# Kernel optimization log

Measured on AMD Instinct MI355X. Metric: run time of the kernel, lower is better.

Reference implementation:

```python
import jax, jax.numpy as jnp
import numpy as np
import math

H = 8        # num_heads
D = 32       # dim_head
DEPTH = 1
LAMBDA_INIT = 0.8 - 0.6 * math.exp(-0.3 * DEPTH)
EPS = 1e-8


def setup_inputs() -> dict:
    key = jax.random.key(0)
    ks = jax.random.split(key, 9)
    B, T, IN_DIM, OUT_DIM = 2, 2048, 1024, 1024
    E = 2 * H * D  # 512
    inp = {
        "x": jax.random.normal(ks[0], (B, T, IN_DIM), dtype=jnp.float32),
        "Wq": jax.random.normal(ks[1], (IN_DIM, E), dtype=jnp.float32) * (IN_DIM ** -0.5),
        "Wkv": jax.random.normal(ks[2], (IN_DIM, 2 * E), dtype=jnp.float32) * (IN_DIM ** -0.5),
        "Wout": jax.random.normal(ks[3], (E, OUT_DIM), dtype=jnp.float32) * (E ** -0.5),
        "lambda_q1": 0.1 * jax.random.normal(ks[4], (D,), dtype=jnp.float32),
        "lambda_k1": 0.1 * jax.random.normal(ks[5], (D,), dtype=jnp.float32),
        "lambda_q2": 0.1 * jax.random.normal(ks[6], (D,), dtype=jnp.float32),
        "lambda_k2": 0.1 * jax.random.normal(ks[7], (D,), dtype=jnp.float32),
        "gamma": jnp.ones((2 * D,), dtype=jnp.float32),
    }
    return inp


def reference(x, Wq, Wkv, Wout, lambda_q1, lambda_k1, lambda_q2, lambda_k2, gamma):
    B, T, _ = x.shape
    scaling = D ** -0.5

    q = (x @ Wq).reshape(B, T, 2 * H, D).transpose(0, 2, 1, 3) * scaling  # [B,2H,T,D]
    kv = x @ Wkv
    k, v = jnp.split(kv, 2, axis=-1)
    k = k.reshape(B, T, 2 * H, D).transpose(0, 2, 1, 3)        # [B,2H,T,D]
    v = v.reshape(B, T, H, 2 * D).transpose(0, 2, 1, 3)        # [B,H,T,2D]

    dots = jnp.einsum('bhqd,bhkd->bhqk', q, k)                 # [B,2H,T,T]
    attn_w = jax.nn.softmax(dots.astype(jnp.float32), axis=-1).astype(dots.dtype)

    lam1 = jnp.exp(jnp.sum(lambda_q1 * lambda_k1))
    lam2 = jnp.exp(jnp.sum(lambda_q2 * lambda_k2))
    lam = lam1 - lam2 + LAMBDA_INIT

    attn_w = attn_w.reshape(B, H, 2, T, T)
    attn_w = attn_w[:, :, 0] - lam * attn_w[:, :, 1]           # [B,H,T,T]

    attn = jnp.einsum('bhqk,bhkd->bhqd', attn_w, v)            # [B,H,T,2D]

    rms = jnp.sqrt(jnp.mean(attn * attn, axis=-1, keepdims=True))
    attn = gamma * (attn / (rms + EPS))
    attn = attn * (1.0 - LAMBDA_INIT)

    attn = attn.transpose(0, 2, 1, 3).reshape(B, T, 2 * H * D)  # [B,T,E]
    return attn @ Wout
```

## Files before the change

kernel.cpp:

```cpp
#include <hip/hip_runtime.h>

typedef __attribute__((ext_vector_type(8)))  _Float16 half8;
typedef __attribute__((ext_vector_type(4)))  _Float16 half4;
typedef __attribute__((ext_vector_type(2)))  __fp16   fp16x2;
typedef __attribute__((ext_vector_type(4)))  float    f32x4;

#define MFMA16(a,b,c) __builtin_amdgcn_mfma_f32_16x16x32_f16(a,b,c,0,0,0)

#define QSCALE       0.17677669529663687f
#define LAMBDA_INIT  0.3555090675909693f
#define OUT_SCALE    0.6444909324090307f
#define LOG2E        1.4426950408889634f
#define MSHIFT       4.0f

#define EXP2(x) __builtin_amdgcn_exp2f(x)

__device__ __forceinline__ void gld16(const void* g, void* l) {
    __builtin_amdgcn_global_load_lds(
        (const __attribute__((address_space(1))) unsigned int*)g,
        (__attribute__((address_space(3))) unsigned int*)l, 16, 0, 0);
}

__device__ __forceinline__ void tr64(const float* __restrict__ src,
                                     _Float16* __restrict__ dst,
                                     int srcld, int dstld, int bx, int by) {
    __shared__ float t[64][65];
    int k0 = bx * 64, n0 = by * 64;
    int c = threadIdx.x & 63, rr = threadIdx.x >> 6;
#pragma unroll
    for (int ph = 0; ph < 16; ++ph) {
        int k = ph * 4 + rr;
        t[k][c] = src[(size_t)(k0 + k) * srcld + n0 + c];
    }
    __syncthreads();
#pragma unroll
    for (int ph = 0; ph < 16; ++ph) {
        int n = ph * 4 + rr;
        dst[(size_t)(n0 + n) * dstld + k0 + c] = (_Float16)t[c][n];
    }
}

__global__ __launch_bounds__(256) void k_prep(const float* __restrict__ x,
                                              const float* __restrict__ Wq,
                                              const float* __restrict__ Wkv,
                                              const float* __restrict__ Wout,
                                              _Float16* __restrict__ xh,
                                              _Float16* __restrict__ WallT,
                                              _Float16* __restrict__ WoutT) {
    int b = blockIdx.x;
    if (b < 4096) {
        int i = (b * 256 + threadIdx.x) * 4;
        f32x4 v = *(const f32x4*)(x + i);
        half4 h;
        h[0] = (_Float16)v[0]; h[1] = (_Float16)v[1];
        h[2] = (_Float16)v[2]; h[3] = (_Float16)v[3];
        *(half4*)(xh + i) = h;
    } else if (b < 4224) {
        int idx = b - 4096;
        tr64(Wq, WallT, 512, 1024, idx & 15, idx >> 4);
    } else if (b < 4480) {
        int idx = b - 4224;
        tr64(Wkv, WallT + 512 * 1024, 1024, 1024, idx & 15, idx >> 4);
    } else {
        int idx = b - 4480;
        tr64(Wout, WoutT, 1024, 512, idx & 7, idx >> 3);
    }
}

__device__ __forceinline__ void gemm_loop(const _Float16* __restrict__ A,
                                          const _Float16* __restrict__ Bt,
                                          int K, int bm, int bn,
                                          char* As, char* Bs,
                                          f32x4 (&acc)[4][4]) {
    int tid = threadIdx.x, lane = tid & 63, w = tid >> 6;
    int col16 = lane & 15, quad = lane >> 4;
    int wm = (w >> 1) << 6, wn = (w & 1) << 6;
    int r0 = tid >> 2;
    int kc = (tid & 3) << 3;
    const _Float16* ga0 = A  + (size_t)(bm + r0) * K + kc;
    const _Float16* ga1 = A  + (size_t)(bm + 64 + r0) * K + kc;
    const _Float16* gb0 = Bt + (size_t)(bn + r0) * K + kc;
    const _Float16* gb1 = Bt + (size_t)(bn + 64 + r0) * K + kc;
    char* lA = As + (w << 10);
    char* lB = Bs + (w << 10);

    gld16(ga0, lA);
    gld16(ga1, lA + 4096);
    gld16(gb0, lB);
    gld16(gb1, lB + 4096);

    for (int k0 = 0; k0 < K; k0 += 32) {
        __syncthreads();
        int cb = (k0 >> 5) & 1;
        if (k0 + 32 < K) {
            int nb = (cb ^ 1) << 13;
            gld16(ga0 + k0 + 32, lA + nb);
            gld16(ga1 + k0 + 32, lA + nb + 4096);
            gld16(gb0 + k0 + 32, lB + nb);
            gld16(gb1 + k0 + 32, lB + nb + 4096);
        }
        const char* Asc = As + (cb << 13);
        const char* Bsc = Bs + (cb << 13);
        half8 af[4], bf[4];
#pragma unroll
        for (int i = 0; i < 4; ++i)
            af[i] = *(const half8*)(Asc + ((wm + i * 16 + col16) << 6) + (quad << 4));
#pragma unroll
        for (int j = 0; j < 4; ++j)
            bf[j] = *(const half8*)(Bsc + ((wn + j * 16 + col16) << 6) + (quad << 4));
#pragma unroll
        for (int i = 0; i < 4; ++i)
#pragma unroll
            for (int j = 0; j < 4; ++j)
                acc[i][j] = MFMA16(af[i], bf[j], acc[i][j]);
    }
}

__global__ __launch_bounds__(256) void k_gemm_qkv(const _Float16* __restrict__ xh,
                                                  const _Float16* __restrict__ WallT,
                                                  _Float16* __restrict__ qbuf,
                                                  char* __restrict__ Kf,
                                                  char* __restrict__ Vf) {
    __shared__ __align__(16) char As[16384];
    __shared__ __align__(16) char Bs[16384];
    f32x4 acc[4][4] = {};
    int bm = blockIdx.x * 128, bn = blockIdx.y * 128;
    gemm_loop(xh, WallT, 1024, bm, bn, As, Bs, acc);

    int tid = threadIdx.x, lane = tid & 63, w = tid >> 6;
    int col16 = lane & 15, quad = lane >> 4;
    int wm = (w >> 1) << 6, wn = (w & 1) << 6;

    if (bn < 512) {
        const float s = QSCALE * LOG2E;
#pragma unroll
        for (int i = 0; i < 4; ++i)
#pragma unroll
            for (int j = 0; j < 4; ++j) {
                int n = bn + wn + j * 16 + col16;
                int m0 = bm + wm + i * 16 + quad * 4;
#pragma unroll
                for (int r = 0; r < 4; ++r)
                    qbuf[(size_t)(m0 + r) * 512 + n] = (_Float16)(acc[i][j][r] * s);
            }
    } else if (bn < 1024) {
#pragma unroll
        for (int j = 0; j < 4; ++j) {
            int n = bn + wn + j * 16 + col16 - 512;
            int pp = n >> 6, dd = n & 63, head = dd >> 5, d32 = dd & 31;
            int lbase = (d32 >> 3) << 4;
            int e2 = (d32 & 7) << 1;
            int fragb = head << 11;
#pragma unroll
            for (int i = 0; i < 4; ++i) {
                int m0 = bm + wm + i * 16 + quad * 4;
                int b = m0 >> 11, tok = m0 & 2047, kb = tok >> 5, kk = tok & 31;
                char* dst = Kf + (((size_t)((b * 8 + pp) * 64 + kb)) << 12)
                          + fragb + ((kk >> 4) << 10) + ((lbase + (kk & 15)) << 4) + e2;
#pragma unroll
                for (int r = 0; r < 4; ++r)
                    *(_Float16*)(dst + (r << 4)) = (_Float16)acc[i][j][r];
            }
        }
    } else {
#pragma unroll
        for (int j = 0; j < 4; ++j) {
            int n = bn + wn + j * 16 + col16 - 1024;
            int pp = n >> 6, ch = n & 63;
            int off_t = ((ch >> 4) << 10) + ((ch & 15) << 4);
#pragma unroll
            for (int i = 0; i < 4; ++i) {
                int m0 = bm + wm + i * 16 + quad * 4;
                int b = m0 >> 11, tok = m0 & 2047, kb = tok >> 5, kk = tok & 31;
                int quadv = (kk < 16) ? (kk >> 2) : ((kk - 16) >> 2);
                int e0 = (kk < 16) ? 0 : 4;
                half4 hv;
#pragma unroll
                for (int r = 0; r < 4; ++r) hv[r] = (_Float16)acc[i][j][r];
                *(half4*)(Vf + (((size_t)((b * 8 + pp) * 64 + kb)) << 12)
                          + off_t + (quadv << 8) + (e0 << 1)) = hv;
            }
        }
    }
}

__global__ __launch_bounds__(512, 4) void k_attn_fused(
        const _Float16* __restrict__ qbuf,
        const char* __restrict__ Kf,
        const char* __restrict__ Vf,
        const float* __restrict__ lq1,
        const float* __restrict__ lk1,
        const float* __restrict__ lq2,
        const float* __restrict__ lk2,
        const float* __restrict__ gamma,
        _Float16* __restrict__ attnO) {
    __shared__ __align__(16) char Sh[2][32768];
    __shared__ float Ls[2][8][16];

    int blk = blockIdx.x;
    int r32 = blk & 63, p = (blk >> 6) & 7, bb = blk >> 9;
    int tid = threadIdx.x, lane = tid & 63, w = tid >> 6;
    int qt2 = w & 1, c = w >> 1;
    int col16 = lane & 15, quad = lane >> 4;

    int qrow = bb * 2048 + r32 * 32 + qt2 * 16 + col16;
    const _Float16* qb = qbuf + (size_t)qrow * 512 + p * 64;
    half8 q1 = *(const half8*)(qb + quad * 8);
    half8 q2 = *(const half8*)(qb + 32 + quad * 8);

    size_t bpoff = ((size_t)(bb * 8 + p)) << 18;
    const char* src2 = ((tid >= 256) ? Vf : Kf) + bpoff + ((tid & 255) << 4);
    int dbase = ((tid >= 256) ? 4096 : 0) + ((tid & 255) << 4);

    const f32x4 minit = {-MSHIFT, -MSHIFT, -MSHIFT, -MSHIFT};

    float l1 = 0.f, l2 = 0.f;
    f32x4 o1[4] = {}, o2[4] = {};

#pragma unroll
    for (int j = 0; j < 4; ++j)
        gld16(src2 + ((size_t)(j << 4) << 12), (char*)Sh + (j << 13) + dbase);

    for (int it = 0; it < 16; ++it) {
        __syncthreads();
        if (it + 1 < 16) {
#pragma unroll
            for (int j = 0; j < 4; ++j)
                gld16(src2 + ((size_t)((j << 4) + it + 1) << 12),
                      (char*)Sh + (((it + 1) & 1) << 15) + (j << 13) + dbase);
        }
        const char* kvb = (char*)Sh + ((it & 1) << 15) + (c << 13) + (lane << 4);

        half8 kf0 = *(const half8*)(kvb);
        half8 kf1 = *(const half8*)(kvb + 1024);
        half8 kf2 = *(const half8*)(kvb + 2048);
        half8 kf3 = *(const half8*)(kvb + 3072);
        f32x4 sa1 = MFMA16(kf0, q1, minit), sb1 = MFMA16(kf1, q1, minit);
        f32x4 sa2 = MFMA16(kf2, q2, minit), sb2 = MFMA16(kf3, q2, minit);

        union { half8 v; fp16x2 h[4]; } p1u, p2u;
        {
            float a0 = EXP2(sa1[0]), a1 = EXP2(sa1[1]);
            float a2 = EXP2(sa1[2]), a3 = EXP2(sa1[3]);
            float b0 = EXP2(sb1[0]), b1 = EXP2(sb1[1]);
            float b2 = EXP2(sb1[2]), b3 = EXP2(sb1[3]);
            l1 += ((a0 + a1) + (a2 + a3)) + ((b0 + b1) + (b2 + b3));
            p1u.h[0] = __builtin_amdgcn_cvt_pkrtz(a0, a1);
            p1u.h[1] = __builtin_amdgcn_cvt_pkrtz(a2, a3);
            p1u.h[2] = __builtin_amdgcn_cvt_pkrtz(b0, b1);
            p1u.h[3] = __builtin_amdgcn_cvt_pkrtz(b2, b3);
        }
        {
            float a0 = EXP2(sa2[0]), a1 = EXP2(sa2[1]);
            float a2 = EXP2(sa2[2]), a3 = EXP2(sa2[3]);
            float b0 = EXP2(sb2[0]), b1 = EXP2(sb2[1]);
            float b2 = EXP2(sb2[2]), b3 = EXP2(sb2[3]);
            l2 += ((a0 + a1) + (a2 + a3)) + ((b0 + b1) + (b2 + b3));
            p2u.h[0] = __builtin_amdgcn_cvt_pkrtz(a0, a1);
            p2u.h[1] = __builtin_amdgcn_cvt_pkrtz(a2, a3);
            p2u.h[2] = __builtin_amdgcn_cvt_pkrtz(b0, b1);
            p2u.h[3] = __builtin_amdgcn_cvt_pkrtz(b2, b3);
        }
        half8 vf0 = *(const half8*)(kvb + 4096);
        half8 vf1 = *(const half8*)(kvb + 5120);
        half8 vf2 = *(const half8*)(kvb + 6144);
        half8 vf3 = *(const half8*)(kvb + 7168);
        o1[0] = MFMA16(p1u.v, vf0, o1[0]); o2[0] = MFMA16(p2u.v, vf0, o2[0]);
        o1[1] = MFMA16(p1u.v, vf1, o1[1]); o2[1] = MFMA16(p2u.v, vf1, o2[1]);
        o1[2] = MFMA16(p1u.v, vf2, o1[2]); o2[2] = MFMA16(p2u.v, vf2, o2[2]);
        o1[3] = MFMA16(p1u.v, vf3, o1[3]); o2[3] = MFMA16(p2u.v, vf3, o2[3]);
    }

    l1 += __shfl_xor(l1, 16); l1 += __shfl_xor(l1, 32);
    l2 += __shfl_xor(l2, 16); l2 += __shfl_xor(l2, 32);

    {
        _Float16* ob = (_Float16*)((char*)Sh + ((c * 2 + qt2) << 12)) + col16;
#pragma unroll
        for (int r = 0; r < 4; ++r) {
            _Float16* od = ob + (quad * 4 + r) * 128;
#pragma unroll
            for (int t = 0; t < 4; ++t) {
                od[t * 16]      = (_Float16)o1[t][r];
                od[64 + t * 16] = (_Float16)o2[t][r];
            }
        }
        if (quad == 0) { Ls[0][w][col16] = l1; Ls[1][w][col16] = l2; }
    }
    __syncthreads();

    int rr = tid >> 4, jj = tid & 15;
    int qrt = rr >> 4, r16 = rr & 15;
    float o1s[4] = {}, o2s[4] = {};
    float l1s = 0.f, l2s = 0.f;
#pragma unroll
    for (int cc = 0; cc < 4; ++cc) {
        const _Float16* ob = (const _Float16*)((char*)Sh + ((cc * 2 + qrt) << 12))
                           + r16 * 128 + jj * 4;
        half4 a  = *(const half4*)ob;
        half4 b2 = *(const half4*)(ob + 64);
#pragma unroll
        for (int e = 0; e < 4; ++e) { o1s[e] += (float)a[e]; o2s[e] += (float)b2[e]; }
        l1s += Ls[0][cc * 2 + qrt][r16];
        l2s += Ls[1][cc * 2 + qrt][r16];
    }
    float s1 = 0.f, s2 = 0.f;
#pragma unroll
    for (int i = 0; i < 32; ++i) { s1 += lq1[i] * lk1[i]; s2 += lq2[i] * lk2[i]; }
    float lam = __expf(s1) - __expf(s2) + LAMBDA_INIT;
    float il1 = 1.f / l1s, il2 = lam / l2s;
    float Of[4], ss = 0.f;
#pragma unroll
    for (int e = 0; e < 4; ++e) { Of[e] = o1s[e] * il1 - o2s[e] * il2; ss += Of[e] * Of[e]; }
    ss += __shfl_xor(ss, 1, 16); ss += __shfl_xor(ss, 2, 16);
    ss += __shfl_xor(ss, 4, 16); ss += __shfl_xor(ss, 8, 16);
    float rms = sqrtf(ss * 0.015625f);
    float sc = OUT_SCALE / (rms + 1e-8f);
    half4 o;
#pragma unroll
    for (int e = 0; e < 4; ++e) o[e] = (_Float16)(gamma[jj * 4 + e] * Of[e] * sc);
    *(half4*)(attnO + ((size_t)(bb * 2048 + r32 * 32 + rr) * 512) + p * 64 + jj * 4) = o;
}

__global__ __launch_bounds__(256) void k_gemm_out(const _Float16* __restrict__ attn,
                                                  const _Float16* __restrict__ WoutT,
                                                  float* __restrict__ out) {
    __shared__ __align__(16) char As[16384];
    __shared__ __align__(16) char Bs[16384];
    f32x4 acc[4][4] = {};
    int bm = blockIdx.x * 128, bn = blockIdx.y * 128;
    gemm_loop(attn, WoutT, 512, bm, bn, As, Bs, acc);

    int tid = threadIdx.x, lane = tid & 63, w = tid >> 6;
    int col16 = lane & 15, quad = lane >> 4;
    int wm = (w >> 1) << 6, wn = (w & 1) << 6;
#pragma unroll
    for (int i = 0; i < 4; ++i)
#pragma unroll
        for (int j = 0; j < 4; ++j) {
            int n = bn + wn + j * 16 + col16;
            int m0 = bm + wm + i * 16 + quad * 4;
#pragma unroll
            for (int r = 0; r < 4; ++r)
                out[(size_t)(m0 + r) * 1024 + n] = acc[i][j][r];
        }
}

extern "C" void kernel_launch(void* const* d_in, const int* in_sizes, int n_in,
                              void* d_out, int out_size, void* d_ws, size_t ws_size,
                              hipStream_t stream) {
    const float* x     = (const float*)d_in[0];
    const float* Wq    = (const float*)d_in[1];
    const float* Wkv   = (const float*)d_in[2];
    const float* Wout  = (const float*)d_in[3];
    const float* lq1   = (const float*)d_in[4];
    const float* lk1   = (const float*)d_in[5];
    const float* lq2   = (const float*)d_in[6];
    const float* lk2   = (const float*)d_in[7];
    const float* gamma = (const float*)d_in[8];
    float* out = (float*)d_out;

    char* ws = (char*)d_ws;
    _Float16* xh    = (_Float16*)(ws);
    _Float16* WallT = (_Float16*)(ws + 8388608);
    _Float16* WoutT = (_Float16*)(ws + 11534336);
    _Float16* qbuf  = (_Float16*)(ws + 12582912);
    char*     Kf    = (char*)(ws + 16777216);
    char*     Vf    = (char*)(ws + 20971520);
    _Float16* attn  = (_Float16*)(ws + 25165824);

    k_prep<<<4608, 256, 0, stream>>>(x, Wq, Wkv, Wout, xh, WallT, WoutT);
    k_gemm_qkv<<<dim3(32, 12), 256, 0, stream>>>(xh, WallT, qbuf, Kf, Vf);
    k_attn_fused<<<1024, 512, 0, stream>>>(qbuf, Kf, Vf, lq1, lk1, lq2, lk2, gamma, attn);
    k_gemm_out<<<dim3(32, 8), 256, 0, stream>>>(attn, WoutT, out);
}
```

Baseline: 168.9 us.

## Load V directly from global to registers, stage only K in LDS, remap blocks

V fragments are now read straight from global memory into registers instead of being staged through LDS. The freed LDS holds twice as many K tiles per stage, so the loop runs 8 iterations over two K sub-tiles each. Block indices are also reordered so that consecutive blocks span different batch/head pairs, which changes the L2 access pattern. The intent is fewer barriers and less LDS traffic per key. The risk is global-load latency on V that is now exposed, plus more registers in use.

After: 175.5 us. 1.04x slower.

```diff
diff --git a/kernel.cpp b/kernel.cpp
--- a/kernel.cpp
+++ b/kernel.cpp
@@ -198,7 +198,9 @@
     __shared__ float Ls[2][8][16];
 
     int blk = blockIdx.x;
-    int r32 = blk & 63, p = (blk >> 6) & 7, bb = blk >> 9;
+    int bp  = ((blk & 7) << 1) | ((blk >> 3) & 1);
+    int r32 = blk >> 4;
+    int p = bp & 7, bb = bp >> 3;
     int tid = threadIdx.x, lane = tid & 63, w = tid >> 6;
     int qt2 = w & 1, c = w >> 1;
     int col16 = lane & 15, quad = lane >> 4;
@@ -209,8 +211,12 @@
     half8 q2 = *(const half8*)(qb + 32 + quad * 8);
 
     size_t bpoff = ((size_t)(bb * 8 + p)) << 18;
-    const char* src2 = ((tid >= 256) ? Vf : Kf) + bpoff + ((tid & 255) << 4);
-    int dbase = ((tid >= 256) ? 4096 : 0) + ((tid & 255) << 4);
+    int j = tid >> 7;
+    int toff = (tid & 127) << 4;
+    const char* ks = Kf + bpoff + ((size_t)j << 16) + toff;
+    int dko = (j << 13) + toff;
+
+    const char* vsrc = Vf + bpoff + ((size_t)c << 16) + (lane << 4);
 
     const f32x4 minit = {-MSHIFT, -MSHIFT, -MSHIFT, -MSHIFT};
 
@@ -218,62 +224,103 @@
     f32x4 o1[4] = {}, o2[4] = {};
 
 #pragma unroll
-    for (int j = 0; j < 4; ++j)
-        gld16(src2 + ((size_t)(j << 4) << 12), (char*)Sh + (j << 13) + dbase);
-
-    for (int it = 0; it < 16; ++it) {
+    for (int r = 0; r < 4; ++r)
+        gld16(ks + r * 2048, (char*)Sh + dko + r * 2048);
+
+    for (int it = 0; it < 8; ++it) {
         __syncthreads();
-        if (it + 1 < 16) {
-#pragma unroll
-            for (int j = 0; j < 4; ++j)
-                gld16(src2 + ((size_t)((j << 4) + it + 1) << 12),
-                      (char*)Sh + (((it + 1) & 1) << 15) + (j << 13) + dbase);
+
+        half8 vA0 = *(const half8*)(vsrc);
+        half8 vA1 = *(const half8*)(vsrc + 1024);
+        half8 vA2 = *(const half8*)(vsrc + 2048);
+        half8 vA3 = *(const half8*)(vsrc + 3072);
+        half8 vB0 = *(const half8*)(vsrc + 4096);
+        half8 vB1 = *(const half8*)(vsrc + 5120);
+        half8 vB2 = *(const half8*)(vsrc + 6144);
+        half8 vB3 = *(const half8*)(vsrc + 7168);
+        vsrc += 8192;
+
+        if (it + 1 < 8) {
+            char* d = (char*)Sh + (((it + 1) & 1) << 15) + dko;
+            const char* s = ks + ((size_t)(it + 1) << 13);
+#pragma unroll
+            for (int r = 0; r < 4; ++r)
+                gld16(s + r * 2048, d + r * 2048);
         }
         const char* kvb = (char*)Sh + ((it & 1) << 15) + (c << 13) + (lane << 4);
 
-        half8 kf0 = *(const half8*)(kvb);
-        half8 kf1 = *(const half8*)(kvb + 1024);
-        half8 kf2 = *(const half8*)(kvb + 2048);
-        half8 kf3 = *(const half8*)(kvb + 3072);
-        f32x4 sa1 = MFMA16(kf0, q1, minit), sb1 = MFMA16(kf1, q1, minit);
-        f32x4 sa2 = MFMA16(kf2, q2, minit), sb2 = MFMA16(kf3, q2, minit);
-
-        union { half8 v; fp16x2 h[4]; } p1u, p2u;
+        half8 ka0 = *(const half8*)(kvb);
+        half8 ka1 = *(const half8*)(kvb + 1024);
+        half8 ka2 = *(const half8*)(kvb + 2048);
+        half8 ka3 = *(const half8*)(kvb + 3072);
+        f32x4 saA1 = MFMA16(ka0, q1, minit), sbA1 = MFMA16(ka1, q1, minit);
+        f32x4 saA2 = MFMA16(ka2, q2, minit), sbA2 = MFMA16(ka3, q2, minit);
+        half8 kb0 = *(const half8*)(kvb + 4096);
+        half8 kb1 = *(const half8*)(kvb + 5120);
+        half8 kb2 = *(const half8*)(kvb + 6144);
+        half8 kb3 = *(const half8*)(kvb + 7168);
+        f32x4 saB1 = MFMA16(kb0, q1, minit), sbB1 = MFMA16(kb1, q1, minit);
+        f32x4 saB2 = MFMA16(kb2, q2, minit), sbB2 = MFMA16(kb3, q2, minit);
+
+        union { half8 v; fp16x2 h[4]; } pA1, pA2, pB1, pB2;
         {
-            float a0 = EXP2(sa1[0]), a1 = EXP2(sa1[1]);
-            float a2 = EXP2(sa1[2]), a3 = EXP2(sa1[3]);
-            float b0 = EXP2(sb1[0]), b1 = EXP2(sb1[1]);
-            float b2 = EXP2(sb1[2]), b3 = EXP2(sb1[3]);
+            float a0 = EXP2(saA1[0]), a1 = EXP2(saA1[1]);
+            float a2 = EXP2(saA1[2]), a3 = EXP2(saA1[3]);
+            float b0 = EXP2(sbA1[0]), b1 = EXP2(sbA1[1]);
+            float b2 = EXP2(sbA1[2]), b3 = EXP2(sbA1[3]);
             l1 += ((a0 + a1) + (a2 + a3)) + ((b0 + b1) + (b2 + b3));
-            p1u.h[0] = __builtin_amdgcn_cvt_pkrtz(a0, a1);
-            p1u.h[1] = __builtin_amdgcn_cvt_pkrtz(a2, a3);
-            p1u.h[2] = __builtin_amdgcn_cvt_pkrtz(b0, b1);
-            p1u.h[3] = __builtin_amdgcn_cvt_pkrtz(b2, b3);
+            pA1.h[0] = __builtin_amdgcn_cvt_pkrtz(a0, a1);
+            pA1.h[1] = __builtin_amdgcn_cvt_pkrtz(a2, a3);
+            pA1.h[2] = __builtin_amdgcn_cvt_pkrtz(b0, b1);
+            pA1.h[3] = __builtin_amdgcn_cvt_pkrtz(b2, b3);
         }
         {
-            float a0 = EXP2(sa2[0]), a1 = EXP2(sa2[1]);
-            float a2 = EXP2(sa2[2]), a3 = EXP2(sa2[3]);
-            float b0 = EXP2(sb2[0]), b1 = EXP2(sb2[1]);
-            float b2 = EXP2(sb2[2]), b3 = EXP2(sb2[3]);
+            float a0 = EXP2(saA2[0]), a1 = EXP2(saA2[1]);
+            float a2 = EXP2(saA2[2]), a3 = EXP2(saA2[3]);
+            float b0 = EXP2(sbA2[0]), b1 = EXP2(sbA2[1]);
+            float b2 = EXP2(sbA2[2]), b3 = EXP2(sbA2[3]);
             l2 += ((a0 + a1) + (a2 + a3)) + ((b0 + b1) + (b2 + b3));
-            p2u.h[0] = __builtin_amdgcn_cvt_pkrtz(a0, a1);
-            p2u.h[1] = __builtin_amdgcn_cvt_pkrtz(a2, a3);
-            p2u.h[2] = __builtin_amdgcn_cvt_pkrtz(b0, b1);
-            p2u.h[3] = __builtin_amdgcn_cvt_pkrtz(b2, b3);
-        }
-        half8 vf0 = *(const half8*)(kvb + 4096);
-        half8 vf1 = *(const half8*)(kvb + 5120);
-        half8 vf2 = *(const half8*)(kvb + 6144);
-        half8 vf3 = *(const half8*)(kvb + 7168);
-        o1[0] = MFMA16(p1u.v, vf0, o1[0]); o2[0] = MFMA16(p2u.v, vf0, o2[0]);
-        o1[1] = MFMA16(p1u.v, vf1, o1[1]); o2[1] = MFMA16(p2u.v, vf1, o2[1]);
-        o1[2] = MFMA16(p1u.v, vf2, o1[2]); o2[2] = MFMA16(p2u.v, vf2, o2[2]);
-        o1[3] = MFMA16(p1u.v, vf3, o1[3]); o2[3] = MFMA16(p2u.v, vf3, o2[3]);
+            pA2.h[0] = __builtin_amdgcn_cvt_pkrtz(a0, a1);
+            pA2.h[1] = __builtin_amdgcn_cvt_pkrtz(a2, a3);
+            pA2.h[2] = __builtin_amdgcn_cvt_pkrtz(b0, b1);
+            pA2.h[3] = __builtin_amdgcn_cvt_pkrtz(b2, b3);
+        }
+        o1[0] = MFMA16(pA1.v, vA0, o1[0]); o2[0] = MFMA16(pA2.v, vA0, o2[0]);
+        o1[1] = MFMA16(pA1.v, vA1, o1[1]); o2[1] = MFMA16(pA2.v, vA1, o2[1]);
+        o1[2] = MFMA16(pA1.v, vA2, o1[2]); o2[2] = MFMA16(pA2.v, vA2, o2[2]);
+        o1[3] = MFMA16(pA1.v, vA3, o1[3]); o2[3] = MFMA16(pA2.v, vA3, o2[3]);
+        {
+            float a0 = EXP2(saB1[0]), a1 = EXP2(saB1[1]);
+            float a2 = EXP2(saB1[2]), a3 = EXP2(saB1[3]);
+            float b0 = EXP2(sbB1[0]), b1 = EXP2(sbB1[1]);
+            float b2 = EXP2(sbB1[2]), b3 = EXP2(sbB1[3]);
+            l1 += ((a0 + a1) + (a2 + a3)) + ((b0 + b1) + (b2 + b3));
+            pB1.h[0] = __builtin_amdgcn_cvt_pkrtz(a0, a1);
+            pB1.h[1] = __builtin_amdgcn_cvt_pkrtz(a2, a3);
+            pB1.h[2] = __builtin_amdgcn_cvt_pkrtz(b0, b1);
+            pB1.h[3] = __builtin_amdgcn_cvt_pkrtz(b2, b3);
+        }
+        {
+            float a0 = EXP2(saB2[0]), a1 = EXP2(saB2[1]);
+            float a2 = EXP2(saB2[2]), a3 = EXP2(saB2[3]);
+            float b0 = EXP2(sbB2[0]), b1 = EXP2(sbB2[1]);
+            float b2 = EXP2(sbB2[2]), b3 = EXP2(sbB2[3]);
+            l2 += ((a0 + a1) + (a2 + a3)) + ((b0 + b1) + (b2 + b3));
+            pB2.h[0] = __builtin_amdgcn_cvt_pkrtz(a0, a1);
+            pB2.h[1] = __builtin_amdgcn_cvt_pkrtz(a2, a3);
+            pB2.h[2] = __builtin_amdgcn_cvt_pkrtz(b0, b1);
+            pB2.h[3] = __builtin_amdgcn_cvt_pkrtz(b2, b3);
+        }
+        o1[0] = MFMA16(pB1.v, vB0, o1[0]); o2[0] = MFMA16(pB2.v, vB0, o2[0]);
+        o1[1] = MFMA16(pB1.v, vB1, o1[1]); o2[1] = MFMA16(pB2.v, vB1, o2[1]);
+        o1[2] = MFMA16(pB1.v, vB2, o1[2]); o2[2] = MFMA16(pB2.v, vB2, o2[2]);
+        o1[3] = MFMA16(pB1.v, vB3, o1[3]); o2[3] = MFMA16(pB2.v, vB3, o2[3]);
     }
 
     l1 += __shfl_xor(l1, 16); l1 += __shfl_xor(l1, 32);
     l2 += __shfl_xor(l2, 16); l2 += __shfl_xor(l2, 32);
 
+    __syncthreads();
     {
         _Float16* ob = (_Float16*)((char*)Sh + ((c * 2 + qt2) << 12)) + col16;
 #pragma unroll
```

## Load V fragments directly from global into registers, stage only K in LDS

Applied to the files above, without the earlier changes.

The attention kernel now stages only K tiles through LDS double buffers, with twice as many keys per iteration (8 iterations instead of 16). V fragments are read straight from global memory into registers at the top of each iteration, so their latency overlaps the K MFMA and exp work. Block index decoding is also changed so that consecutive blocks cover different (batch, head) pairs, which spreads L2 traffic. A barrier is added before the epilogue reuses the shared buffer. In exchange, V loads are no longer shared through LDS, so they add global and L2 traffic and register pressure.

After: 167.8 us. About the same (-0.7%).

```diff
diff --git a/kernel.cpp b/kernel.cpp
--- a/kernel.cpp
+++ b/kernel.cpp
@@ -198,7 +198,9 @@
     __shared__ float Ls[2][8][16];
 
     int blk = blockIdx.x;
-    int r32 = blk & 63, p = (blk >> 6) & 7, bb = blk >> 9;
+    int bp  = ((blk & 7) << 1) | ((blk >> 3) & 1);
+    int r32 = blk >> 4;
+    int p = bp & 7, bb = bp >> 3;
     int tid = threadIdx.x, lane = tid & 63, w = tid >> 6;
     int qt2 = w & 1, c = w >> 1;
     int col16 = lane & 15, quad = lane >> 4;
@@ -209,8 +211,12 @@
     half8 q2 = *(const half8*)(qb + 32 + quad * 8);
 
     size_t bpoff = ((size_t)(bb * 8 + p)) << 18;
-    const char* src2 = ((tid >= 256) ? Vf : Kf) + bpoff + ((tid & 255) << 4);
-    int dbase = ((tid >= 256) ? 4096 : 0) + ((tid & 255) << 4);
+    int j = tid >> 7;
+    int toff = (tid & 127) << 4;
+    const char* ks = Kf + bpoff + ((size_t)j << 16) + toff;
+    int dko = (j << 13) + toff;
+
+    const char* vsrc = Vf + bpoff + ((size_t)c << 16) + (lane << 4);
 
     const f32x4 minit = {-MSHIFT, -MSHIFT, -MSHIFT, -MSHIFT};
 
@@ -218,62 +224,82 @@
     f32x4 o1[4] = {}, o2[4] = {};
 
 #pragma unroll
-    for (int j = 0; j < 4; ++j)
-        gld16(src2 + ((size_t)(j << 4) << 12), (char*)Sh + (j << 13) + dbase);
-
-    for (int it = 0; it < 16; ++it) {
+    for (int r = 0; r < 4; ++r)
+        gld16(ks + r * 2048, (char*)Sh + dko + r * 2048);
+
+    for (int it = 0; it < 8; ++it) {
         __syncthreads();
-        if (it + 1 < 16) {
-#pragma unroll
-            for (int j = 0; j < 4; ++j)
-                gld16(src2 + ((size_t)((j << 4) + it + 1) << 12),
-                      (char*)Sh + (((it + 1) & 1) << 15) + (j << 13) + dbase);
+
+        half8 vA0 = *(const half8*)(vsrc);
+        half8 vA1 = *(const half8*)(vsrc + 1024);
+        half8 vA2 = *(const half8*)(vsrc + 2048);
+        half8 vA3 = *(const half8*)(vsrc + 3072);
+        half8 vB0 = *(const half8*)(vsrc + 4096);
+        half8 vB1 = *(const half8*)(vsrc + 5120);
+        half8 vB2 = *(const half8*)(vsrc + 6144);
+        half8 vB3 = *(const half8*)(vsrc + 7168);
+        vsrc += 8192;
+
+        if (it + 1 < 8) {
+            char* d = (char*)Sh + (((it + 1) & 1) << 15) + dko;
+            const char* s = ks + ((size_t)(it + 1) << 13);
+#pragma unroll
+            for (int r = 0; r < 4; ++r)
+                gld16(s + r * 2048, d + r * 2048);
         }
         const char* kvb = (char*)Sh + ((it & 1) << 15) + (c << 13) + (lane << 4);
 
-        half8 kf0 = *(const half8*)(kvb);
-        half8 kf1 = *(const half8*)(kvb + 1024);
-        half8 kf2 = *(const half8*)(kvb + 2048);
-        half8 kf3 = *(const half8*)(kvb + 3072);
-        f32x4 sa1 = MFMA16(kf0, q1, minit), sb1 = MFMA16(kf1, q1, minit);
-        f32x4 sa2 = MFMA16(kf2, q2, minit), sb2 = MFMA16(kf3, q2, minit);
-
-        union { half8 v; fp16x2 h[4]; } p1u, p2u;
-        {
-            float a0 = EXP2(sa1[0]), a1 = EXP2(sa1[1]);
-            float a2 = EXP2(sa1[2]), a3 = EXP2(sa1[3]);
-            float b0 = EXP2(sb1[0]), b1 = EXP2(sb1[1]);
-            float b2 = EXP2(sb1[2]), b3 = EXP2(sb1[3]);
-            l1 += ((a0 + a1) + (a2 + a3)) + ((b0 + b1) + (b2 + b3));
-            p1u.h[0] = __builtin_amdgcn_cvt_pkrtz(a0, a1);
-            p1u.h[1] = __builtin_amdgcn_cvt_pkrtz(a2, a3);
-            p1u.h[2] = __builtin_amdgcn_cvt_pkrtz(b0, b1);
-            p1u.h[3] = __builtin_amdgcn_cvt_pkrtz(b2, b3);
-        }
-        {
-            float a0 = EXP2(sa2[0]), a1 = EXP2(sa2[1]);
-            float a2 = EXP2(sa2[2]), a3 = EXP2(sa2[3]);
-            float b0 = EXP2(sb2[0]), b1 = EXP2(sb2[1]);
-            float b2 = EXP2(sb2[2]), b3 = EXP2(sb2[3]);
-            l2 += ((a0 + a1) + (a2 + a3)) + ((b0 + b1) + (b2 + b3));
-            p2u.h[0] = __builtin_amdgcn_cvt_pkrtz(a0, a1);
-            p2u.h[1] = __builtin_amdgcn_cvt_pkrtz(a2, a3);
-            p2u.h[2] = __builtin_amdgcn_cvt_pkrtz(b0, b1);
-            p2u.h[3] = __builtin_amdgcn_cvt_pkrtz(b2, b3);
-        }
-        half8 vf0 = *(const half8*)(kvb + 4096);
-        half8 vf1 = *(const half8*)(kvb + 5120);
-        half8 vf2 = *(const half8*)(kvb + 6144);
-        half8 vf3 = *(const half8*)(kvb + 7168);
-        o1[0] = MFMA16(p1u.v, vf0, o1[0]); o2[0] = MFMA16(p2u.v, vf0, o2[0]);
-        o1[1] = MFMA16(p1u.v, vf1, o1[1]); o2[1] = MFMA16(p2u.v, vf1, o2[1]);
-        o1[2] = MFMA16(p1u.v, vf2, o1[2]); o2[2] = MFMA16(p2u.v, vf2, o2[2]);
-        o1[3] = MFMA16(p1u.v, vf3, o1[3]); o2[3] = MFMA16(p2u.v, vf3, o2[3]);
+#pragma unroll
+        for (int h = 0; h < 2; ++h) {
+            const char* kh = kvb + (h << 12);
+            half8 kf0 = *(const half8*)(kh);
+            half8 kf1 = *(const half8*)(kh + 1024);
+            half8 kf2 = *(const half8*)(kh + 2048);
+            half8 kf3 = *(const half8*)(kh + 3072);
+            f32x4 sa1 = MFMA16(kf0, q1, minit), sb1 = MFMA16(kf1, q1, minit);
+            f32x4 sa2 = MFMA16(kf2, q2, minit), sb2 = MFMA16(kf3, q2, minit);
+
+            union { half8 v; fp16x2 h[4]; } p1u, p2u;
+            {
+                float a0 = EXP2(sa1[0]), a1 = EXP2(sa1[1]);
+                float a2 = EXP2(sa1[2]), a3 = EXP2(sa1[3]);
+                float b0 = EXP2(sb1[0]), b1 = EXP2(sb1[1]);
+                float b2 = EXP2(sb1[2]), b3 = EXP2(sb1[3]);
+                l1 += ((a0 + a1) + (a2 + a3)) + ((b0 + b1) + (b2 + b3));
+                p1u.h[0] = __builtin_amdgcn_cvt_pkrtz(a0, a1);
+                p1u.h[1] = __builtin_amdgcn_cvt_pkrtz(a2, a3);
+                p1u.h[2] = __builtin_amdgcn_cvt_pkrtz(b0, b1);
+                p1u.h[3] = __builtin_amdgcn_cvt_pkrtz(b2, b3);
+            }
+            {
+                float a0 = EXP2(sa2[0]), a1 = EXP2(sa2[1]);
+                float a2 = EXP2(sa2[2]), a3 = EXP2(sa2[3]);
+                float b0 = EXP2(sb2[0]), b1 = EXP2(sb2[1]);
+                float b2 = EXP2(sb2[2]), b3 = EXP2(sb2[3]);
+                l2 += ((a0 + a1) + (a2 + a3)) + ((b0 + b1) + (b2 + b3));
+                p2u.h[0] = __builtin_amdgcn_cvt_pkrtz(a0, a1);
+                p2u.h[1] = __builtin_amdgcn_cvt_pkrtz(a2, a3);
+                p2u.h[2] = __builtin_amdgcn_cvt_pkrtz(b0, b1);
+                p2u.h[3] = __builtin_amdgcn_cvt_pkrtz(b2, b3);
+            }
+            if (h == 0) {
+                o1[0] = MFMA16(p1u.v, vA0, o1[0]); o2[0] = MFMA16(p2u.v, vA0, o2[0]);
+                o1[1] = MFMA16(p1u.v, vA1, o1[1]); o2[1] = MFMA16(p2u.v, vA1, o2[1]);
+                o1[2] = MFMA16(p1u.v, vA2, o1[2]); o2[2] = MFMA16(p2u.v, vA2, o2[2]);
+                o1[3] = MFMA16(p1u.v, vA3, o1[3]); o2[3] = MFMA16(p2u.v, vA3, o2[3]);
+            } else {
+                o1[0] = MFMA16(p1u.v, vB0, o1[0]); o2[0] = MFMA16(p2u.v, vB0, o2[0]);
+                o1[1] = MFMA16(p1u.v, vB1, o1[1]); o2[1] = MFMA16(p2u.v, vB1, o2[1]);
+                o1[2] = MFMA16(p1u.v, vB2, o1[2]); o2[2] = MFMA16(p2u.v, vB2, o2[2]);
+                o1[3] = MFMA16(p1u.v, vB3, o1[3]); o2[3] = MFMA16(p2u.v, vB3, o2[3]);
+            }
+        }
     }
 
     l1 += __shfl_xor(l1, 16); l1 += __shfl_xor(l1, 32);
     l2 += __shfl_xor(l2, 16); l2 += __shfl_xor(l2, 32);
 
+    __syncthreads();
     {
         _Float16* ob = (_Float16*)((char*)Sh + ((c * 2 + qt2) << 12)) + col16;
 #pragma unroll
```
